# Kernel optimization log

Measured on AMD Instinct MI355X. Metric: run time of the kernel, lower is better.

Reference implementation:

```python
import jax, jax.numpy as jnp
import numpy as np

N = 50000   # nodes
E = 1600000 # edges
NF = 128    # input features
H = 128     # hidden
C = 40      # classes
EPS = 1e-5


def setup_inputs() -> dict:
    key = jax.random.key(0)
    ks = jax.random.split(key, 8)
    s_in = 1.0 / np.sqrt(NF)
    s_h = 1.0 / np.sqrt(H)
    return {
        "x": jax.random.normal(ks[0], (N, NF), jnp.float32),
        "edge_index": jax.random.randint(ks[1], (2, E), 0, N, dtype=jnp.int32),
        "W1": jax.random.normal(ks[2], (NF, H), jnp.float32) * s_in,
        "b1": jnp.zeros((H,), jnp.float32),
        "W2": jax.random.normal(ks[3], (H, H), jnp.float32) * s_h,
        "b2": jnp.zeros((H,), jnp.float32),
        "W3": jax.random.normal(ks[4], (H, H), jnp.float32) * s_h,
        "b3": jnp.zeros((H,), jnp.float32),
        "g1": jnp.ones((H,), jnp.float32), "be1": jnp.zeros((H,), jnp.float32),
        "g2": jnp.ones((H,), jnp.float32), "be2": jnp.zeros((H,), jnp.float32),
        "g3": jnp.ones((H,), jnp.float32), "be3": jnp.zeros((H,), jnp.float32),
        "fcW": jax.random.normal(ks[5], (H, C), jnp.float32) * s_h,
        "fcb": jnp.zeros((C,), jnp.float32),
    }


def _bn(x, g, b):
    # BatchNorm1d training-mode semantics: batch mean / biased batch var
    m = jnp.mean(x, axis=0)
    v = jnp.mean(jnp.square(x - m), axis=0)
    return g * (x - m) * jax.lax.rsqrt(v + EPS) + b


def reference(x, edge_index, W1, b1, W2, b2, W3, b3,
              g1, be1, g2, be2, g3, be3, fcW, fcb):
    n = x.shape[0]
    loop = jnp.arange(n, dtype=edge_index.dtype)
    src = jnp.concatenate([edge_index[0], loop])  # [E+N]
    dst = jnp.concatenate([edge_index[1], loop])
    # symmetric GCN normalization with self-loops
    deg = jax.ops.segment_sum(jnp.ones_like(src, dtype=x.dtype), dst, num_segments=n)
    dis = jnp.where(deg > 0, jax.lax.rsqrt(jnp.maximum(deg, 1.0)), 0.0)
    norm = dis[src] * dis[dst]  # [E+N]

    def conv(h, W, b):
        hw = h @ W  # [n, H]
        msg = hw[src] * norm[:, None]  # [E+N, H] gather + scale
        return jax.ops.segment_sum(msg, dst, num_segments=n) + b  # scatter-add

    h = jax.nn.relu(_bn(conv(x, W1, b1), g1, be1))
    h = jax.nn.relu(_bn(conv(h, W2, b2), g2, be2))  # dropout: eval mode (identity)
    h = jax.nn.relu(_bn(conv(h, W3, b3), g3, be3))
    logits = jax.nn.relu(h @ fcW + fcb)
    return jax.nn.log_softmax(logits, axis=1), logits
```

## Files before the change

### kernel.cpp

```cpp
#include <hip/hip_runtime.h>
#include <hip/hip_bf16.h>
#include <math.h>

#define NODES 50000
#define EDGES 1600000
#define HD    128
#define NC    40
#define EPSV  1e-5f
#define NBKT  196
#define CSRMAX 12032

typedef unsigned int uint;
typedef unsigned short ushort;
typedef __attribute__((ext_vector_type(8))) short bfrag;
typedef __attribute__((ext_vector_type(4))) float ffrag;

union FragU { uint4 u; bfrag f; };

__device__ inline ushort bf1(float x) {
  uint u = __float_as_uint(x);
  return (ushort)((u + 0x7fffu + ((u >> 16) & 1u)) >> 16);
}
__device__ inline uint bf2(float a, float b) {
  return (uint)bf1(a) | ((uint)bf1(b) << 16);
}
__device__ inline float ulo(uint u) { return __uint_as_float(u << 16); }
__device__ inline float uhi(uint u) { return __uint_as_float(u & 0xffff0000u); }


__global__ __launch_bounds__(256)
void k_bcount(const int* __restrict__ dst, int* __restrict__ bcnt, int e_) {
  __shared__ int h[256];
  int t = threadIdx.x;
  h[t] = 0;
  __syncthreads();
  int base = blockIdx.x * 8192;
  int cntE = min(8192, e_ - base);
  for (int i = t; i < cntE; i += 256) atomicAdd(&h[dst[base + i] >> 8], 1);
  __syncthreads();
  if (h[t]) atomicAdd(&bcnt[t], h[t]);
}

__global__ void k_bscan(const int* __restrict__ bcnt, int* __restrict__ bbase,
                        int* __restrict__ bcur, int* __restrict__ row_ptr) {
  __shared__ int s[256];
  int t = threadIdx.x;
  int v = bcnt[t];
  s[t] = v;
  __syncthreads();
#pragma unroll
  for (int off = 1; off < 256; off <<= 1) {
    int y = (t >= off) ? s[t - off] : 0;
    __syncthreads();
    s[t] += y;
    __syncthreads();
  }
  int excl = s[t] - v;
  bbase[t] = excl;
  bcur[t] = excl;
  if (t == 255) {
    bbase[256] = s[255];
    row_ptr[NODES] = s[255];
  }
}

__global__ __launch_bounds__(256)
void k_bin(const int* __restrict__ src, const int* __restrict__ dst,
           int* __restrict__ bcur, uint* __restrict__ staging, int e_) {
  __shared__ uint ent[8192];
  __shared__ int h[256], inc[256], lofs[256], cur[256], gb[256];
  int t = threadIdx.x;
  h[t] = 0;
  __syncthreads();
  int base = blockIdx.x * 8192;
  int cntE = min(8192, e_ - base);
  for (int i = t; i < cntE; i += 256) atomicAdd(&h[dst[base + i] >> 8], 1);
  __syncthreads();
  inc[t] = h[t];
  __syncthreads();
#pragma unroll
  for (int off = 1; off < 256; off <<= 1) {
    int y = (t >= off) ? inc[t - off] : 0;
    __syncthreads();
    inc[t] += y;
    __syncthreads();
  }
  lofs[t] = inc[t] - h[t];
  cur[t] = 0;
  __syncthreads();
  for (int i = t; i < cntE; i += 256) {
    int e = base + i;
    int d = dst[e];
    int b = d >> 8;
    uint en = (uint)(src[e] & 0xffff) | ((uint)(d & 255) << 16) | ((uint)b << 24);
    int p = lofs[b] + atomicAdd(&cur[b], 1);
    ent[p] = en;
  }
  __syncthreads();
  if (h[t]) gb[t] = atomicAdd(&bcur[t], h[t]);
  __syncthreads();
  for (int i = t; i < cntE; i += 256) {
    uint en = ent[i];
    int b = en >> 24;
    staging[gb[b] + (i - lofs[b])] = en;
  }
}

__global__ __launch_bounds__(256)
void k_csr(const uint* __restrict__ staging, const int* __restrict__ bbase,
           ushort* __restrict__ csr, int* __restrict__ row_ptr,
           float* __restrict__ dis, int n) {
  __shared__ uint ent[CSRMAX];
  __shared__ ushort srt[CSRMAX];
  __shared__ int cnt_[256], ofs_[256], cur_[256];
  int b = blockIdx.x, t = threadIdx.x;
  int base = bbase[b];
  int cnt = bbase[b + 1] - base;
  if (cnt > CSRMAX) cnt = CSRMAX;
  for (int i = t; i < cnt; i += 256) ent[i] = staging[base + i];
  cnt_[t] = 0;
  __syncthreads();
  for (int i = t; i < cnt; i += 256) atomicAdd(&cnt_[(ent[i] >> 16) & 255], 1);
  __syncthreads();
  ofs_[t] = cnt_[t];
  __syncthreads();
#pragma unroll
  for (int off = 1; off < 256; off <<= 1) {
    int y = (t >= off) ? ofs_[t - off] : 0;
    __syncthreads();
    ofs_[t] += y;
    __syncthreads();
  }
  int myofs = ofs_[t] - cnt_[t];
  ofs_[t] = myofs;
  cur_[t] = 0;
  __syncthreads();
  int node = (b << 8) + t;
  if (node < n) {
    row_ptr[node] = base + myofs;
    dis[node] = rsqrtf((float)(cnt_[t] + 1));
  }
  for (int i = t; i < cnt; i += 256) {
    uint e = ent[i];
    int dl = (e >> 16) & 255;
    int p = ofs_[dl] + atomicAdd(&cur_[dl], 1);
    srt[p] = (ushort)(e & 0xffff);
  }
  __syncthreads();
  for (int i = t; i < cnt; i += 256) csr[base + i] = srt[i];
}

__global__ void k_prepw(const float* __restrict__ W1, const float* __restrict__ W2,
                        const float* __restrict__ W3, const float* __restrict__ fcW,
                        ushort* __restrict__ wt) {
  int idx = blockIdx.x * 256 + threadIdx.x;
  if (idx < 49152) {
    int r = idx >> 14;
    int i = idx & 16383;
    int nn = i >> 7, k = i & 127;
    const float* W = (r == 0) ? W1 : ((r == 1) ? W2 : W3);
    wt[idx] = bf1(W[k * 128 + nn]);
  } else if (idx < 55296) {
    int i = idx - 49152;
    int nn = i >> 7, k = i & 127;
    wt[idx] = (nn < NC) ? bf1(fcW[k * NC + nn]) : (ushort)0;
  }
}

__device__ inline void bn_prologue(const float* __restrict__ part,
                                   const float* __restrict__ g,
                                   const float* __restrict__ be,
                                   float* s_scale, float* s_shift) {
  __shared__ float tmp[256];
  int t = threadIdx.x;
  float s = 0.f;
#pragma unroll 8
  for (int p = 0; p < 64; ++p) s += part[p * 256 + t];
  tmp[t] = s;
  __syncthreads();
  if (t < 128) {
    const float inv_n = 1.0f / (float)NODES;
    float m = tmp[t] * inv_n;
    float var = tmp[128 + t] * inv_n - m * m;
    float rstd = rsqrtf(var + EPSV);
    float sc = g[t] * rstd;
    s_scale[t] = sc;
    s_shift[t] = be[t] - m * sc;
  }
  __syncthreads();
}

template<int MODE>
__global__ __launch_bounds__(256)
void k_gemm_mx(const void* __restrict__ Ain, const uint* __restrict__ Wt,
               ushort* __restrict__ Cb, int n,
               const float* __restrict__ part, const float* __restrict__ g,
               const float* __restrict__ be) {
  __shared__ float s_scale[128], s_shift[128];
  if (MODE == 1) bn_prologue(part, g, be, s_scale, s_shift);

  const int lane = threadIdx.x & 63;
  const int wave = threadIdx.x >> 6;
  const int quad = lane >> 4;
  const int ml = lane & 15;
  const int row0 = blockIdx.x * 64 + wave * 16;
  const int arow = row0 + ml;
  ffrag acc[8];
#pragma unroll
  for (int i = 0; i < 8; ++i) acc[i] = (ffrag){0.f, 0.f, 0.f, 0.f};

#pragma unroll
  for (int s = 0; s < 4; ++s) {
    const int k0 = s * 32 + quad * 8;
    FragU a;
    if (arow < n) {
      if (MODE == 1) {
        const uint* Ab = (const uint*)Ain;
        uint4 v = *(const uint4*)&Ab[(size_t)arow * 64 + (k0 >> 1)];
        float4 sc0 = *(const float4*)&s_scale[k0];
        float4 sc1 = *(const float4*)&s_scale[k0 + 4];
        float4 sh0 = *(const float4*)&s_shift[k0];
        float4 sh1 = *(const float4*)&s_shift[k0 + 4];
        a.u.x = bf2(fmaxf(fmaf(ulo(v.x), sc0.x, sh0.x), 0.f), fmaxf(fmaf(uhi(v.x), sc0.y, sh0.y), 0.f));
        a.u.y = bf2(fmaxf(fmaf(ulo(v.y), sc0.z, sh0.z), 0.f), fmaxf(fmaf(uhi(v.y), sc0.w, sh0.w), 0.f));
        a.u.z = bf2(fmaxf(fmaf(ulo(v.z), sc1.x, sh1.x), 0.f), fmaxf(fmaf(uhi(v.z), sc1.y, sh1.y), 0.f));
        a.u.w = bf2(fmaxf(fmaf(ulo(v.w), sc1.z, sh1.z), 0.f), fmaxf(fmaf(uhi(v.w), sc1.w, sh1.w), 0.f));
      } else {
        const float* Af = (const float*)Ain;
        float4 a0 = *(const float4*)&Af[(size_t)arow * 128 + k0];
        float4 a1 = *(const float4*)&Af[(size_t)arow * 128 + k0 + 4];
        a.u.x = bf2(a0.x, a0.y);
        a.u.y = bf2(a0.z, a0.w);
        a.u.z = bf2(a1.x, a1.y);
        a.u.w = bf2(a1.z, a1.w);
      }
    } else {
      a.u = make_uint4(0, 0, 0, 0);
    }
#pragma unroll
    for (int nt = 0; nt < 8; ++nt) {
      FragU b;
      b.u = *(const uint4*)&Wt[(size_t)(nt * 16 + ml) * 64 + (k0 >> 1)];
      acc[nt] = __builtin_amdgcn_mfma_f32_16x16x32_bf16(a.f, b.f, acc[nt], 0, 0, 0);
    }
  }
#pragma unroll
  for (int nt = 0; nt < 8; ++nt) {
#pragma unroll
    for (int r = 0; r < 4; ++r) {
      int orow = row0 + quad * 4 + r;
      if (orow < n) Cb[(size_t)orow * 128 + nt * 16 + ml] = bf1(acc[nt][r]);
    }
  }
}

__global__ __launch_bounds__(256)
void k_agg(const uint* __restrict__ t, const int* __restrict__ row_ptr,
           const ushort* __restrict__ csr, const float* __restrict__ dis,
           uint* __restrict__ hb, float* __restrict__ part, int n) {
  __shared__ float red[4][256];
  int node = (blockIdx.x * 256 + threadIdx.x) >> 6;
  int lane = threadIdx.x & 63;
  int wave = threadIdx.x >> 6;
  int quarter = lane >> 4;
  int fl = lane & 15;
  int e0 = row_ptr[node], e1 = row_ptr[node + 1];
  float dd = dis[node];
  float acc[8] = {};

  for (int chunk = e0; chunk < e1; chunk += 64) {
    int m = min(64, e1 - chunk);
    int s = 0;
    float w = 0.f;
    if (lane < m) {
      s = csr[chunk + lane];
      w = dis[s] * dd;
    }
#pragma unroll 2
    for (int j = 0; j < m; j += 8) {
      int j0 = j + quarter, j1 = j + 4 + quarter;
      int s0 = __shfl(s, j0, 64), s1 = __shfl(s, j1, 64);
      float w0 = __shfl(w, j0, 64), w1 = __shfl(w, j1, 64);
      bool p0 = j0 < m, p1 = j1 < m;
      uint4 v0 = make_uint4(0, 0, 0, 0), v1 = make_uint4(0, 0, 0, 0);
      if (p0) v0 = *(const uint4*)&t[(size_t)s0 * 64 + (fl << 2)];
      if (p1) v1 = *(const uint4*)&t[(size_t)s1 * 64 + (fl << 2)];
      if (p0) {
        acc[0] = fmaf(w0, ulo(v0.x), acc[0]);
        acc[1] = fmaf(w0, uhi(v0.x), acc[1]);
        acc[2] = fmaf(w0, ulo(v0.y), acc[2]);
        acc[3] = fmaf(w0, uhi(v0.y), acc[3]);
        acc[4] = fmaf(w0, ulo(v0.z), acc[4]);
        acc[5] = fmaf(w0, uhi(v0.z), acc[5]);
        acc[6] = fmaf(w0, ulo(v0.w), acc[6]);
        acc[7] = fmaf(w0, uhi(v0.w), acc[7]);
      }
      if (p1) {
        acc[0] = fmaf(w1, ulo(v1.x), acc[0]);
        acc[1] = fmaf(w1, uhi(v1.x), acc[1]);
        acc[2] = fmaf(w1, ulo(v1.y), acc[2]);
        acc[3] = fmaf(w1, uhi(v1.y), acc[3]);
        acc[4] = fmaf(w1, ulo(v1.z), acc[4]);
        acc[5] = fmaf(w1, uhi(v1.z), acc[5]);
        acc[6] = fmaf(w1, ulo(v1.w), acc[6]);
        acc[7] = fmaf(w1, uhi(v1.w), acc[7]);
      }
    }
  }
#pragma unroll
  for (int j = 0; j < 8; ++j) {
    acc[j] += __shfl_xor(acc[j], 16, 64);
    acc[j] += __shfl_xor(acc[j], 32, 64);
  }
  if (quarter == 0) {
    float d2 = dd * dd;
    uint4 v = *(const uint4*)&t[(size_t)node * 64 + (fl << 2)];
    acc[0] = fmaf(d2, ulo(v.x), acc[0]);
    acc[1] = fmaf(d2, uhi(v.x), acc[1]);
    acc[2] = fmaf(d2, ulo(v.y), acc[2]);
    acc[3] = fmaf(d2, uhi(v.y), acc[3]);
    acc[4] = fmaf(d2, ulo(v.z), acc[4]);
    acc[5] = fmaf(d2, uhi(v.z), acc[5]);
    acc[6] = fmaf(d2, ulo(v.w), acc[6]);
    acc[7] = fmaf(d2, uhi(v.w), acc[7]);
    uint4 o;
    o.x = bf2(acc[0], acc[1]);
    o.y = bf2(acc[2], acc[3]);
    o.z = bf2(acc[4], acc[5]);
    o.w = bf2(acc[6], acc[7]);
    *(uint4*)&hb[(size_t)node * 64 + (fl << 2)] = o;
    *(float4*)&red[wave][fl * 8]     = make_float4(acc[0], acc[1], acc[2], acc[3]);
    *(float4*)&red[wave][fl * 8 + 4] = make_float4(acc[4], acc[5], acc[6], acc[7]);
  }
  __syncthreads();
  int tt = threadIdx.x;
  if (tt < 128) {
    float s = red[0][tt] + red[1][tt] + red[2][tt] + red[3][tt];
    atomicAdd(&part[(blockIdx.x & 63) * 256 + tt], s);
  } else {
    int f = tt - 128;
    float s = red[0][f] * red[0][f] + red[1][f] * red[1][f] +
              red[2][f] * red[2][f] + red[3][f] * red[3][f];
    atomicAdd(&part[(blockIdx.x & 63) * 256 + tt], s);
  }
}

__global__ __launch_bounds__(256)
void k_fc_mx(const uint* __restrict__ hb, const float* __restrict__ part,
             const float* __restrict__ g, const float* __restrict__ be,
             const uint* __restrict__ fWt, const float* __restrict__ fcb,
             float* __restrict__ out, int n) {
  __shared__ float s_scale[128], s_shift[128];
  bn_prologue(part, g, be, s_scale, s_shift);

  const int lane = threadIdx.x & 63;
  const int wave = threadIdx.x >> 6;
  const int quad = lane >> 4;
  const int ml = lane & 15;
  const int row0 = blockIdx.x * 64 + wave * 16;
  const int arow = row0 + ml;
  ffrag acc[3];
#pragma unroll
  for (int i = 0; i < 3; ++i) acc[i] = (ffrag){0.f, 0.f, 0.f, 0.f};

#pragma unroll
  for (int s = 0; s < 4; ++s) {
    const int k0 = s * 32 + quad * 8;
    FragU a;
    if (arow < n) {
      uint4 v = *(const uint4*)&hb[(size_t)arow * 64 + (k0 >> 1)];
      float4 sc0 = *(const float4*)&s_scale[k0];
      float4 sc1 = *(const float4*)&s_scale[k0 + 4];
      float4 sh0 = *(const float4*)&s_shift[k0];
      float4 sh1 = *(const float4*)&s_shift[k0 + 4];
      a.u.x = bf2(fmaxf(fmaf(ulo(v.x), sc0.x, sh0.x), 0.f), fmaxf(fmaf(uhi(v.x), sc0.y, sh0.y), 0.f));
      a.u.y = bf2(fmaxf(fmaf(ulo(v.y), sc0.z, sh0.z), 0.f), fmaxf(fmaf(uhi(v.y), sc0.w, sh0.w), 0.f));
      a.u.z = bf2(fmaxf(fmaf(ulo(v.z), sc1.x, sh1.x), 0.f), fmaxf(fmaf(uhi(v.z), sc1.y, sh1.y), 0.f));
      a.u.w = bf2(fmaxf(fmaf(ulo(v.w), sc1.z, sh1.z), 0.f), fmaxf(fmaf(uhi(v.w), sc1.w, sh1.w), 0.f));
    } else {
      a.u = make_uint4(0, 0, 0, 0);
    }
#pragma unroll
    for (int nt = 0; nt < 3; ++nt) {
      FragU b;
      b.u = *(const uint4*)&fWt[(size_t)(nt * 16 + ml) * 64 + (k0 >> 1)];
      acc[nt] = __builtin_amdgcn_mfma_f32_16x16x32_bf16(a.f, b.f, acc[nt], 0, 0, 0);
    }
  }

  float b0 = fcb[ml], b1 = fcb[16 + ml];
  float b2 = (ml < 8) ? fcb[32 + ml] : 0.f;
#pragma unroll
  for (int r = 0; r < 4; ++r) {
    int orow = row0 + quad * 4 + r;
    if (orow >= n) continue;
    float l0 = fmaxf(acc[0][r] + b0, 0.f);
    float l1 = fmaxf(acc[1][r] + b1, 0.f);
    float l2 = (ml < 8) ? fmaxf(acc[2][r] + b2, 0.f) : -1e30f;
    float mx = fmaxf(fmaxf(l0, l1), l2);
#pragma unroll
    for (int off = 1; off < 16; off <<= 1) mx = fmaxf(mx, __shfl_xor(mx, off, 64));
    float sm = __expf(l0 - mx) + __expf(l1 - mx) + ((ml < 8) ? __expf(l2 - mx) : 0.f);
#pragma unroll
    for (int off = 1; off < 16; off <<= 1) sm += __shfl_xor(sm, off, 64);
    float lse = mx + __logf(sm);
    float* o1 = out + (size_t)orow * NC;
    float* o2 = out + (size_t)NODES * NC + (size_t)orow * NC;
    o1[ml] = l0 - lse;
    o1[16 + ml] = l1 - lse;
    o2[ml] = l0;
    o2[16 + ml] = l1;
    if (ml < 8) {
      o1[32 + ml] = l2 - lse;
      o2[32 + ml] = l2;
    }
  }
}


extern "C" void kernel_launch(void* const* d_in, const int* in_sizes, int n_in,
                              void* d_out, int out_size, void* d_ws, size_t ws_size,
                              hipStream_t stream) {
  (void)in_sizes; (void)n_in; (void)out_size; (void)ws_size;
  const float* x   = (const float*)d_in[0];
  const int*   ei  = (const int*)d_in[1];
  const float* W1  = (const float*)d_in[2];
  const float* W2  = (const float*)d_in[4];
  const float* W3  = (const float*)d_in[6];
  const float* g1  = (const float*)d_in[8];
  const float* be1 = (const float*)d_in[9];
  const float* g2  = (const float*)d_in[10];
  const float* be2 = (const float*)d_in[11];
  const float* g3  = (const float*)d_in[12];
  const float* be3 = (const float*)d_in[13];
  const float* fcW = (const float*)d_in[14];
  const float* fcb = (const float*)d_in[15];
  float* out = (float*)d_out;

  const int n = NODES, e_ = EDGES;
  const int* srcp = ei;
  const int* dstp = ei + e_;

  char* ws = (char*)d_ws;
  size_t off = 0;
  auto alloc = [&](size_t bytes) {
    char* p = ws + off;
    off = (off + bytes + 255) & ~(size_t)255;
    return p;
  };
  float* dis    = (float*)alloc((size_t)n * 4);
  int*   bcnt   = (int*)  alloc(256 * 4);
  float* parts  = (float*)alloc(3 * 64 * 256 * 4);
  int*   bbase  = (int*)  alloc(257 * 4);
  int*   bcur   = (int*)  alloc(256 * 4);
  int*   row_ptr= (int*)  alloc((size_t)(n + 1) * 4);
  uint*  staging= (uint*) alloc((size_t)e_ * 4);
  ushort* csr   = (ushort*)alloc((size_t)e_ * 2);
  uint*  tbuf   = (uint*) alloc((size_t)n * 64 * 4);
  uint*  hbuf   = (uint*) alloc((size_t)n * 64 * 4);
  ushort* wbuf  = (ushort*)alloc(55296 * 2);

  const uint* Wt1  = (const uint*)wbuf;
  const uint* Wt2  = (const uint*)wbuf + 8192;
  const uint* Wt3  = (const uint*)wbuf + 16384;
  const uint* fWt  = (const uint*)wbuf + 24576;

  const int ebk = (e_ + 8191) / 8192;

  hipMemsetAsync(bcnt, 0, 256 * 4 + 3 * 64 * 256 * 4, stream);
  k_bcount<<<ebk, 256, 0, stream>>>(dstp, bcnt, e_);
  k_bscan<<<1, 256, 0, stream>>>(bcnt, bbase, bcur, row_ptr);
  k_bin<<<ebk, 256, 0, stream>>>(srcp, dstp, bcur, staging, e_);
  k_csr<<<NBKT, 256, 0, stream>>>(staging, bbase, csr, row_ptr, dis, n);
  k_prepw<<<216, 256, 0, stream>>>(W1, W2, W3, fcW, wbuf);

  const int ggrid = (n + 63) / 64;
  float* p0 = parts;
  float* p1 = parts + 64 * 256;
  float* p2 = parts + 2 * 64 * 256;

  k_gemm_mx<0><<<ggrid, 256, 0, stream>>>(x, Wt1, (ushort*)tbuf, n, nullptr, nullptr, nullptr);
  k_agg<<<n / 4, 256, 0, stream>>>(tbuf, row_ptr, csr, dis, hbuf, p0, n);
  k_gemm_mx<1><<<ggrid, 256, 0, stream>>>(hbuf, Wt2, (ushort*)tbuf, n, p0, g1, be1);
  k_agg<<<n / 4, 256, 0, stream>>>(tbuf, row_ptr, csr, dis, hbuf, p1, n);
  k_gemm_mx<1><<<ggrid, 256, 0, stream>>>(hbuf, Wt3, (ushort*)tbuf, n, p1, g2, be2);
  k_agg<<<n / 4, 256, 0, stream>>>(tbuf, row_ptr, csr, dis, hbuf, p2, n);
  k_fc_mx<<<ggrid, 256, 0, stream>>>(hbuf, p2, g3, be3, fWt, fcb, out, n);
}
```

Baseline: 397.6 us.

## Precompute packed edge weights and split aggregation across feature column blocks

Adds a one-time kernel that packs each CSR source index with its bf16 normalization weight into a 32-bit word, so the aggregation kernels no longer gather dis[src] per edge. The aggregation grid gains a second dimension of 4 feature slices of 32 columns. Each wave now handles 16 edges at a time, reading 64 bytes per neighbor row instead of 256. This aims to cut dependent dis gathers and raise memory-level parallelism, at the cost of rounding the edge weights to bf16, re-reading the CSR 4 times per layer, and a larger reduction shuffle.

```diff
diff --git a/kernel.cpp b/kernel.cpp
--- a/kernel.cpp
+++ b/kernel.cpp
@@ -148,6 +148,21 @@
   }
   __syncthreads();
   for (int i = t; i < cnt; i += 256) csr[base + i] = srt[i];
+}
+
+__global__ __launch_bounds__(256)
+void k_wfill(const ushort* __restrict__ csr, const int* __restrict__ row_ptr,
+             const float* __restrict__ dis, uint* __restrict__ csrw, int n) {
+  int node = blockIdx.x * 4 + (threadIdx.x >> 6);
+  if (node >= n) return;
+  int lane = threadIdx.x & 63;
+  int e0 = row_ptr[node], e1 = row_ptr[node + 1];
+  float dd = dis[node];
+  for (int e = e0 + lane; e < e1; e += 64) {
+    int s = csr[e];
+    float w = dis[s] * dd;
+    csrw[e] = (uint)s | ((uint)bf1(w) << 16);
+  }
 }
 
 __global__ void k_prepw(const float* __restrict__ W1, const float* __restrict__ W2,
@@ -256,35 +271,33 @@
 
 __global__ __launch_bounds__(256)
 void k_agg(const uint* __restrict__ t, const int* __restrict__ row_ptr,
-           const ushort* __restrict__ csr, const float* __restrict__ dis,
+           const uint* __restrict__ csrw, const float* __restrict__ dis,
            uint* __restrict__ hb, float* __restrict__ part, int n) {
-  __shared__ float red[4][256];
-  int node = (blockIdx.x * 256 + threadIdx.x) >> 6;
+  __shared__ float redS[4][32], redQ[4][32];
+  int node = blockIdx.x * 4 + (threadIdx.x >> 6);
   int lane = threadIdx.x & 63;
   int wave = threadIdx.x >> 6;
-  int quarter = lane >> 4;
-  int fl = lane & 15;
+  int grp = lane >> 2;
+  int fl = lane & 3;
+  const int c16 = blockIdx.y << 4;
   int e0 = row_ptr[node], e1 = row_ptr[node + 1];
-  float dd = dis[node];
   float acc[8] = {};
 
   for (int chunk = e0; chunk < e1; chunk += 64) {
     int m = min(64, e1 - chunk);
-    int s = 0;
-    float w = 0.f;
-    if (lane < m) {
-      s = csr[chunk + lane];
-      w = dis[s] * dd;
-    }
+    uint ev = 0;
+    if (lane < m) ev = csrw[chunk + lane];
 #pragma unroll 2
-    for (int j = 0; j < m; j += 8) {
-      int j0 = j + quarter, j1 = j + 4 + quarter;
-      int s0 = __shfl(s, j0, 64), s1 = __shfl(s, j1, 64);
-      float w0 = __shfl(w, j0, 64), w1 = __shfl(w, j1, 64);
+    for (int j = 0; j < m; j += 32) {
+      int j0 = j + grp, j1 = j + 16 + grp;
+      uint ev0 = __shfl(ev, j0, 64);
+      uint ev1 = __shfl(ev, j1, 64);
       bool p0 = j0 < m, p1 = j1 < m;
       uint4 v0 = make_uint4(0, 0, 0, 0), v1 = make_uint4(0, 0, 0, 0);
-      if (p0) v0 = *(const uint4*)&t[(size_t)s0 * 64 + (fl << 2)];
-      if (p1) v1 = *(const uint4*)&t[(size_t)s1 * 64 + (fl << 2)];
+      if (p0) v0 = *(const uint4*)&t[(size_t)(ev0 & 0xffffu) * 64 + c16 + (fl << 2)];
+      if (p1) v1 = *(const uint4*)&t[(size_t)(ev1 & 0xffffu) * 64 + c16 + (fl << 2)];
+      float w0 = __uint_as_float(ev0 & 0xffff0000u);
+      float w1 = __uint_as_float(ev1 & 0xffff0000u);
       if (p0) {
         acc[0] = fmaf(w0, ulo(v0.x), acc[0]);
         acc[1] = fmaf(w0, uhi(v0.x), acc[1]);
@@ -309,12 +322,15 @@
   }
 #pragma unroll
   for (int j = 0; j < 8; ++j) {
+    acc[j] += __shfl_xor(acc[j], 4, 64);
+    acc[j] += __shfl_xor(acc[j], 8, 64);
     acc[j] += __shfl_xor(acc[j], 16, 64);
     acc[j] += __shfl_xor(acc[j], 32, 64);
   }
-  if (quarter == 0) {
+  if (grp == 0) {
+    float dd = dis[node];
     float d2 = dd * dd;
-    uint4 v = *(const uint4*)&t[(size_t)node * 64 + (fl << 2)];
+    uint4 v = *(const uint4*)&t[(size_t)node * 64 + c16 + (fl << 2)];
     acc[0] = fmaf(d2, ulo(v.x), acc[0]);
     acc[1] = fmaf(d2, uhi(v.x), acc[1]);
     acc[2] = fmaf(d2, ulo(v.y), acc[2]);
@@ -328,20 +344,22 @@
     o.y = bf2(acc[2], acc[3]);
     o.z = bf2(acc[4], acc[5]);
     o.w = bf2(acc[6], acc[7]);
-    *(uint4*)&hb[(size_t)node * 64 + (fl << 2)] = o;
-    *(float4*)&red[wave][fl * 8]     = make_float4(acc[0], acc[1], acc[2], acc[3]);
-    *(float4*)&red[wave][fl * 8 + 4] = make_float4(acc[4], acc[5], acc[6], acc[7]);
+    *(uint4*)&hb[(size_t)node * 64 + c16 + (fl << 2)] = o;
+#pragma unroll
+    for (int j = 0; j < 8; ++j) {
+      redS[wave][fl * 8 + j] = acc[j];
+      redQ[wave][fl * 8 + j] = acc[j] * acc[j];
+    }
   }
   __syncthreads();
   int tt = threadIdx.x;
-  if (tt < 128) {
-    float s = red[0][tt] + red[1][tt] + red[2][tt] + red[3][tt];
-    atomicAdd(&part[(blockIdx.x & 63) * 256 + tt], s);
-  } else {
-    int f = tt - 128;
-    float s = red[0][f] * red[0][f] + red[1][f] * red[1][f] +
-              red[2][f] * red[2][f] + red[3][f] * red[3][f];
-    atomicAdd(&part[(blockIdx.x & 63) * 256 + tt], s);
+  if (tt < 32) {
+    float s = redS[0][tt] + redS[1][tt] + redS[2][tt] + redS[3][tt];
+    atomicAdd(&part[(blockIdx.x & 63) * 256 + (blockIdx.y << 5) + tt], s);
+  } else if (tt < 64) {
+    int f = tt - 32;
+    float s = redQ[0][f] + redQ[1][f] + redQ[2][f] + redQ[3][f];
+    atomicAdd(&part[(blockIdx.x & 63) * 256 + 128 + (blockIdx.y << 5) + f], s);
   }
 }
 
@@ -456,6 +474,7 @@
   int*   row_ptr= (int*)  alloc((size_t)(n + 1) * 4);
   uint*  staging= (uint*) alloc((size_t)e_ * 4);
   ushort* csr   = (ushort*)alloc((size_t)e_ * 2);
+  uint*  csrw   = (uint*) alloc((size_t)e_ * 4);
   uint*  tbuf   = (uint*) alloc((size_t)n * 64 * 4);
   uint*  hbuf   = (uint*) alloc((size_t)n * 64 * 4);
   ushort* wbuf  = (ushort*)alloc(55296 * 2);
@@ -472,18 +491,20 @@
   k_bscan<<<1, 256, 0, stream>>>(bcnt, bbase, bcur, row_ptr);
   k_bin<<<ebk, 256, 0, stream>>>(srcp, dstp, bcur, staging, e_);
   k_csr<<<NBKT, 256, 0, stream>>>(staging, bbase, csr, row_ptr, dis, n);
+  k_wfill<<<n / 4, 256, 0, stream>>>(csr, row_ptr, dis, csrw, n);
   k_prepw<<<216, 256, 0, stream>>>(W1, W2, W3, fcW, wbuf);
 
   const int ggrid = (n + 63) / 64;
+  const dim3 agrid(n / 4, 4);
   float* p0 = parts;
   float* p1 = parts + 64 * 256;
   float* p2 = parts + 2 * 64 * 256;
 
   k_gemm_mx<0><<<ggrid, 256, 0, stream>>>(x, Wt1, (ushort*)tbuf, n, nullptr, nullptr, nullptr);
-  k_agg<<<n / 4, 256, 0, stream>>>(tbuf, row_ptr, csr, dis, hbuf, p0, n);
+  k_agg<<<agrid, 256, 0, stream>>>(tbuf, row_ptr, csrw, dis, hbuf, p0, n);
   k_gemm_mx<1><<<ggrid, 256, 0, stream>>>(hbuf, Wt2, (ushort*)tbuf, n, p0, g1, be1);
-  k_agg<<<n / 4, 256, 0, stream>>>(tbuf, row_ptr, csr, dis, hbuf, p1, n);
+  k_agg<<<agrid, 256, 0, stream>>>(tbuf, row_ptr, csrw, dis, hbuf, p1, n);
   k_gemm_mx<1><<<ggrid, 256, 0, stream>>>(hbuf, Wt3, (ushort*)tbuf, n, p1, g2, be2);
-  k_agg<<<n / 4, 256, 0, stream>>>(tbuf, row_ptr, csr, dis, hbuf, p2, n);
+  k_agg<<<agrid, 256, 0, stream>>>(tbuf, row_ptr, csrw, dis, hbuf, p2, n);
   k_fc_mx<<<ggrid, 256, 0, stream>>>(hbuf, p2, g3, be3, fWt, fcb, out, n);
 }
```

Measured after the change: 543.0 us. 1.37x slower.
